# Optimization experiments

Measured on AMD Instinct MI355X. Metric: run time of the kernel, lower is better.

## Reference

```python
import jax, jax.numpy as jnp
import numpy as np

N_NODES = 100000


def gcn_conv(x, W, b, src, dst, n):
    """PyG GCNConv: add self-loops, symmetric degree norm, linear, scatter-add."""
    loop = jnp.arange(n, dtype=src.dtype)
    s = jnp.concatenate([src, loop])  # source nodes (message origin)
    d = jnp.concatenate([dst, loop])  # target nodes (aggregation)
    deg = jax.ops.segment_sum(jnp.ones_like(d, dtype=x.dtype), d, num_segments=n)
    dinv = jnp.where(deg > 0, jax.lax.rsqrt(deg), 0.0)
    norm = dinv[s] * dinv[d]  # [E+N]
    h = x @ W  # [N, out]
    msg = h[s] * norm[:, None]  # [E+N, out]
    return jax.ops.segment_sum(msg, d, num_segments=n) + b


def setup_inputs() -> dict:
    key = jax.random.key(0)
    ks = jax.random.split(key, 8)
    n, e, din, dh, dout = N_NODES, 3200000, 128, 64, 6
    x = jax.random.normal(ks[0], (n, din), dtype=jnp.float32)
    edge_index = jax.random.randint(ks[1], (2, e), 0, n, dtype=jnp.int64)
    sc = lambda f: 1.0 / np.sqrt(f)
    W1 = jax.random.normal(ks[2], (din, dh), dtype=jnp.float32) * sc(din)
    b1 = jnp.zeros((dh,), dtype=jnp.float32)
    W2 = jax.random.normal(ks[3], (dh, dh), dtype=jnp.float32) * sc(dh)
    b2 = jnp.zeros((dh,), dtype=jnp.float32)
    W3 = jax.random.normal(ks[4], (dh, dout), dtype=jnp.float32) * sc(dh)
    b3 = jnp.zeros((dout,), dtype=jnp.float32)
    return {"x": x, "edge_index": edge_index, "W1": W1, "b1": b1,
            "W2": W2, "b2": b2, "W3": W3, "b3": b3}


def reference(x, edge_index, W1, b1, W2, b2, W3, b3):
    n = x.shape[0]
    src, dst = edge_index[0], edge_index[1]
    # eval mode: dropout is identity
    h = jax.nn.relu(gcn_conv(x, W1, b1, src, dst, n))
    h = jax.nn.relu(gcn_conv(h, W2, b2, src, dst, n))
    h = gcn_conv(h, W3, b3, src, dst, n)
    return jax.nn.log_softmax(h, axis=1)
```

## Files before the change

### kernel.cpp

```cpp
#include <hip/hip_runtime.h>
#include <hip/hip_fp16.h>
#include <math.h>


#define WS_ALIGN(x) (((x) + 255) & ~(size_t)255)
#define BKN 256
#define CAP 8960
#define EPT 16
#define BIN_THR 512
#define BIN_CHUNK (BIN_THR * EPT)

typedef _Float16 half8 __attribute__((ext_vector_type(8)));
typedef float floatx4 __attribute__((ext_vector_type(4)));

__global__ __launch_bounds__(BIN_THR) void bin_kernel(
    const int* __restrict__ src, const int* __restrict__ dst,
    int* __restrict__ cur, int* __restrict__ slab, int E, int NB) {
    __shared__ int counts[400];
    const int tid = threadIdx.x;
    const int base = blockIdx.x * BIN_CHUNK + tid * EPT;
    for (int i = tid; i < NB; i += BIN_THR) counts[i] = 0;
    __syncthreads();
    int b[EPT], w[EPT], lpos[EPT];
    #pragma unroll
    for (int k = 0; k < EPT; ++k) {
        int e = base + k;
        if (e < E) {
            int s = src[e], d = dst[e];
            b[k] = d >> 8;
            w[k] = (s << 8) | (d & 255);
        } else b[k] = -1;
    }
    #pragma unroll
    for (int k = 0; k < EPT; ++k)
        if (b[k] >= 0) lpos[k] = atomicAdd(&counts[b[k]], 1);
    __syncthreads();
    for (int i = tid; i < NB; i += BIN_THR) {
        int c = counts[i];
        counts[i] = c ? atomicAdd(&cur[i], c) : 0;
    }
    __syncthreads();
    #pragma unroll
    for (int k = 0; k < EPT; ++k) {
        if (b[k] >= 0) {
            int pos = counts[b[k]] + lpos[k];
            if (pos < CAP) slab[(size_t)b[k] * CAP + pos] = w[k];
        }
    }
}

__global__ __launch_bounds__(512) void bucket_sort_kernel(
    const int* __restrict__ slab, const int* __restrict__ cur,
    int* __restrict__ srcS, int* __restrict__ rowbeg, int* __restrict__ rowend,
    float* __restrict__ dinv, int n) {
    __shared__ int cnt[BKN], s[BKN], cursor[BKN];
    const int b = blockIdx.x, tid = threadIdx.x;
    const int m = min(cur[b], CAP);
    const int* sp = slab + (size_t)b * CAP;
    if (tid < BKN) cnt[tid] = 0;
    __syncthreads();
    for (int j = tid; j < m; j += 512) atomicAdd(&cnt[sp[j] & 255], 1);
    __syncthreads();
    if (tid < BKN) s[tid] = cnt[tid];
    __syncthreads();
    for (int off = 1; off < BKN; off <<= 1) {
        int v = 0;
        if (tid < BKN && tid >= off) v = s[tid - off];
        __syncthreads();
        if (tid < BKN) s[tid] += v;
        __syncthreads();
    }
    if (tid < BKN) {
        int ofs = s[tid] - cnt[tid];
        cursor[tid] = ofs;
        int node = b * BKN + tid;
        if (node < n) {
            rowbeg[node] = b * CAP + ofs;
            rowend[node] = b * CAP + ofs + cnt[tid];
            dinv[node] = rsqrtf((float)(cnt[tid] + 1));
        }
    }
    __syncthreads();
    for (int j = tid; j < m; j += 512) {
        int w = sp[j];
        int p = atomicAdd(&cursor[w & 255], 1);
        srcS[(size_t)b * CAP + p] = w >> 8;
    }
}

template <int K>
__global__ __launch_bounds__(256) void linear_mfma_f32_kernel(
    const float* __restrict__ Xf, const float* __restrict__ W,
    const float* __restrict__ dinv, _Float16* __restrict__ Y, int n) {
    constexpr int KC = K / 32;
    __shared__ _Float16 Bf[KC * 4 * 64 * 8];
    const int tid = threadIdx.x;
    for (int i = tid; i < KC * 4 * 64 * 8; i += 256) {
        int j = i & 7, lane = (i >> 3) & 63, tile = (i >> 9) & 3, kc = i >> 11;
        int k = kc * 32 + ((lane >> 4) << 3) + j;
        int col = tile * 16 + (lane & 15);
        Bf[i] = (_Float16)W[k * 64 + col];
    }
    __syncthreads();
    const int lane = tid & 63, wid = tid >> 6;
    const int base = blockIdx.x * 64 + wid * 16;
    if (base >= n) return;
    const int mrow = lane & 15, quad = lane >> 4;
    const int anode = min(base + mrow, n - 1);
    floatx4 acc[4] = {{0, 0, 0, 0}, {0, 0, 0, 0}, {0, 0, 0, 0}, {0, 0, 0, 0}};
    #pragma unroll
    for (int kc = 0; kc < KC; ++kc) {
        float4 xa = *(const float4*)&Xf[(size_t)anode * K + kc * 32 + quad * 8];
        float4 xb = *(const float4*)&Xf[(size_t)anode * K + kc * 32 + quad * 8 + 4];
        half8 a;
        a[0] = (_Float16)xa.x; a[1] = (_Float16)xa.y; a[2] = (_Float16)xa.z; a[3] = (_Float16)xa.w;
        a[4] = (_Float16)xb.x; a[5] = (_Float16)xb.y; a[6] = (_Float16)xb.z; a[7] = (_Float16)xb.w;
        #pragma unroll
        for (int t = 0; t < 4; ++t) {
            half8 b = *(const half8*)&Bf[((kc * 4 + t) * 64 + lane) * 8];
            acc[t] = __builtin_amdgcn_mfma_f32_16x16x32_f16(a, b, acc[t], 0, 0, 0);
        }
    }
    #pragma unroll
    for (int r = 0; r < 4; ++r) {
        int node = base + quad * 4 + r;
        if (node < n) {
            float di = dinv[node];
            #pragma unroll
            for (int t = 0; t < 4; ++t)
                Y[(size_t)node * 64 + t * 16 + mrow] = (_Float16)(acc[t][r] * di);
        }
    }
}

__global__ __launch_bounds__(256) void linear_mfma_f16_kernel(
    const _Float16* __restrict__ Xh, const float* __restrict__ W,
    const float* __restrict__ dinv, _Float16* __restrict__ Y, int n) {
    constexpr int K = 64, KC = 2;
    __shared__ _Float16 Bf[KC * 4 * 64 * 8];
    const int tid = threadIdx.x;
    for (int i = tid; i < KC * 4 * 64 * 8; i += 256) {
        int j = i & 7, lane = (i >> 3) & 63, tile = (i >> 9) & 3, kc = i >> 11;
        int k = kc * 32 + ((lane >> 4) << 3) + j;
        int col = tile * 16 + (lane & 15);
        Bf[i] = (_Float16)W[k * 64 + col];
    }
    __syncthreads();
    const int lane = tid & 63, wid = tid >> 6;
    const int base = blockIdx.x * 64 + wid * 16;
    if (base >= n) return;
    const int mrow = lane & 15, quad = lane >> 4;
    const int anode = min(base + mrow, n - 1);
    floatx4 acc[4] = {{0, 0, 0, 0}, {0, 0, 0, 0}, {0, 0, 0, 0}, {0, 0, 0, 0}};
    #pragma unroll
    for (int kc = 0; kc < KC; ++kc) {
        half8 a = *(const half8*)&Xh[(size_t)anode * K + kc * 32 + quad * 8];
        #pragma unroll
        for (int t = 0; t < 4; ++t) {
            half8 b = *(const half8*)&Bf[((kc * 4 + t) * 64 + lane) * 8];
            acc[t] = __builtin_amdgcn_mfma_f32_16x16x32_f16(a, b, acc[t], 0, 0, 0);
        }
    }
    #pragma unroll
    for (int r = 0; r < 4; ++r) {
        int node = base + quad * 4 + r;
        if (node < n) {
            float di = dinv[node];
            #pragma unroll
            for (int t = 0; t < 4; ++t)
                Y[(size_t)node * 64 + t * 16 + mrow] = (_Float16)(acc[t][r] * di);
        }
    }
}

__global__ __launch_bounds__(256) void linear3_kernel(const __half* __restrict__ Xh,
                                                      const float* __restrict__ W,
                                                      const float* __restrict__ dinv,
                                                      __half* __restrict__ Y, int n) {
    __shared__ float Wl[64 * 6];
    __shared__ float Xs[32][65];
    const int tid = threadIdx.x;
    for (int i = tid; i < 64 * 6; i += 256) Wl[i] = W[i];
    const int sub = tid >> 3;
    const int feat = tid & 7;
    for (int base = blockIdx.x * 32; base < n; base += gridDim.x * 32) {
        __syncthreads();
        for (int i = tid; i < 32 * 64; i += 256) {
            int r = i >> 6, c = i & 63;
            int node = base + r;
            Xs[r][c] = (node < n) ? __half2float(Xh[(size_t)node * 64 + c]) : 0.f;
        }
        __syncthreads();
        int node = base + sub;
        if (node < n) {
            float r = 0.f;
            if (feat < 6) {
                float acc = 0.f;
                #pragma unroll
                for (int k = 0; k < 64; ++k) acc = fmaf(Xs[sub][k], Wl[k * 6 + feat], acc);
                r = acc * dinv[node];
            }
            Y[(size_t)node * 8 + feat] = __float2half_rn(r);
        }
    }
}

__global__ __launch_bounds__(256) void agg64_kernel(
    const _Float16* __restrict__ Hs, const float* __restrict__ dinv,
    const int* __restrict__ srcS, const int* __restrict__ rowbeg,
    const int* __restrict__ rowend, const float* __restrict__ bias,
    _Float16* __restrict__ Out, int n, int do_relu) {
    const int wave = (blockIdx.x * blockDim.x + threadIdx.x) >> 6;
    const int lane = threadIdx.x & 63;
    if (wave >= n) return;
    const int slot = lane >> 3;
    const int f8 = lane & 7;
    const int beg = rowbeg[wave], end = rowend[wave];
    float acc[8] = {0.f, 0.f, 0.f, 0.f, 0.f, 0.f, 0.f, 0.f};
    int j = beg;
    for (; j + 16 <= end; j += 16) {
        int sA = srcS[j + slot];
        int sB = srcS[j + 8 + slot];
        half8 vA = *(const half8*)&Hs[(size_t)sA * 64 + f8 * 8];
        half8 vB = *(const half8*)&Hs[(size_t)sB * 64 + f8 * 8];
        #pragma unroll
        for (int i = 0; i < 8; ++i) acc[i] += (float)vA[i] + (float)vB[i];
    }
    for (; j < end; j += 8) {
        int jj = j + slot;
        int s = srcS[min(jj, end - 1)];
        half8 v = *(const half8*)&Hs[(size_t)s * 64 + f8 * 8];
        float flag = (jj < end) ? 1.f : 0.f;
        #pragma unroll
        for (int i = 0; i < 8; ++i) acc[i] = fmaf((float)v[i], flag, acc[i]);
    }
    #pragma unroll
    for (int i = 0; i < 8; ++i) {
        acc[i] += __shfl_xor(acc[i], 8);
        acc[i] += __shfl_xor(acc[i], 16);
        acc[i] += __shfl_xor(acc[i], 32);
    }
    half8 self = *(const half8*)&Hs[(size_t)wave * 64 + f8 * 8];
    const float di = dinv[wave];
    float4 b0 = *(const float4*)&bias[f8 * 8];
    float4 b1 = *(const float4*)&bias[f8 * 8 + 4];
    float bb[8] = {b0.x, b0.y, b0.z, b0.w, b1.x, b1.y, b1.z, b1.w};
    half8 o;
    #pragma unroll
    for (int i = 0; i < 8; ++i) {
        float v = (acc[i] + (float)self[i]) * di + bb[i];
        if (do_relu) v = fmaxf(v, 0.f);
        o[i] = (_Float16)v;
    }
    if (slot == 0) *(half8*)&Out[(size_t)wave * 64 + f8 * 8] = o;
}

__global__ __launch_bounds__(256) void agg6_lsm_kernel(
    const __half* __restrict__ Hs6, const float* __restrict__ dinv,
    const int* __restrict__ srcS, const int* __restrict__ rowbeg,
    const int* __restrict__ rowend, const float* __restrict__ bias,
    float* __restrict__ out, int n) {
    const int wave = (blockIdx.x * blockDim.x + threadIdx.x) >> 6;
    const int lane = threadIdx.x & 63;
    if (wave >= n) return;
    const int slot = lane >> 3, f = lane & 7;
    const int beg = rowbeg[wave], end = rowend[wave];
    float part = 0.f;
    for (int j0 = beg; j0 < end; j0 += 8) {
        int j = j0 + slot;
        if (j < end) part += __half2float(Hs6[(size_t)srcS[j] * 8 + f]);
    }
    part += __shfl_xor(part, 8);
    part += __shfl_xor(part, 16);
    part += __shfl_xor(part, 32);
    float bi = (f < 6) ? bias[f] : 0.f;
    float a = (part + __half2float(Hs6[(size_t)wave * 8 + f])) * dinv[wave] + bi;
    float am = (f < 6) ? a : -1e30f;
    float m = am;
    m = fmaxf(m, __shfl_xor(m, 1));
    m = fmaxf(m, __shfl_xor(m, 2));
    m = fmaxf(m, __shfl_xor(m, 4));
    float ex = (f < 6) ? expf(a - m) : 0.f;
    float sum = ex;
    sum += __shfl_xor(sum, 1);
    sum += __shfl_xor(sum, 2);
    sum += __shfl_xor(sum, 4);
    float lse = m + logf(sum);
    if (slot == 0 && f < 6) out[(size_t)wave * 6 + f] = a - lse;
}

extern "C" void kernel_launch(void* const* d_in, const int* in_sizes, int n_in,
                              void* d_out, int out_size, void* d_ws, size_t ws_size,
                              hipStream_t stream) {
    const float* x  = (const float*)d_in[0];
    const int*   ei = (const int*)d_in[1];
    const float* W1 = (const float*)d_in[2];
    const float* b1 = (const float*)d_in[3];
    const float* W2 = (const float*)d_in[4];
    const float* b2 = (const float*)d_in[5];
    const float* W3 = (const float*)d_in[6];
    const float* b3 = (const float*)d_in[7];
    float* out = (float*)d_out;

    const int n = in_sizes[0] / 128;
    const int E = in_sizes[1] / 2;
    const int* src = ei;
    const int* dst = ei + E;
    const int NB = (n + BKN - 1) / BKN;

    char* ws = (char*)d_ws;
    auto carve = [&](size_t bytes) { char* p = ws; ws += WS_ALIGN(bytes); return p; };
    int*      cur    = (int*)     carve((size_t)NB * 4);
    float*    dinv   = (float*)   carve((size_t)n * 4);
    int*      slab   = (int*)     carve((size_t)NB * CAP * 4);
    int*      srcS   = (int*)     carve((size_t)NB * CAP * 4);
    int*      rowbeg = (int*)     carve((size_t)n * 4);
    int*      rowend = (int*)     carve((size_t)n * 4);
    _Float16* hsA    = (_Float16*)carve((size_t)n * 64 * 2 + 4096);
    _Float16* hsB    = (_Float16*)carve((size_t)n * 64 * 2 + 4096);
    __half*   hsC    = (__half*)  carve((size_t)n * 8 * 2);
    (void)ws_size; (void)n_in; (void)out_size;

    hipMemsetAsync(cur, 0, (size_t)NB * 4, stream);
    bin_kernel<<<(E + BIN_CHUNK - 1) / BIN_CHUNK, BIN_THR, 0, stream>>>(src, dst, cur, slab, E, NB);
    bucket_sort_kernel<<<NB, 512, 0, stream>>>(slab, cur, srcS, rowbeg, rowend, dinv, n);

    const int aggGrid = (n + 3) / 4;
    const int linGrid = (n + 63) / 64;

    linear_mfma_f32_kernel<128><<<linGrid, 256, 0, stream>>>(x, W1, dinv, hsA, n);
    agg64_kernel<<<aggGrid, 256, 0, stream>>>(hsA, dinv, srcS, rowbeg, rowend, b1, hsB, n, 1);

    linear_mfma_f16_kernel<<<linGrid, 256, 0, stream>>>(hsB, W2, dinv, hsA, n);
    agg64_kernel<<<aggGrid, 256, 0, stream>>>(hsA, dinv, srcS, rowbeg, rowend, b2, hsB, n, 1);

    linear3_kernel<<<2048, 256, 0, stream>>>((const __half*)hsB, W3, dinv, hsC, n);
    agg6_lsm_kernel<<<aggGrid, 256, 0, stream>>>(hsC, dinv, srcS, rowbeg, rowend, b3, out, n);
}
```

Measured before the change: 374.3 us.

## Accumulate aggregation in packed fp16, shrink buckets, pack row bounds into int2

The aggregation kernel now sums neighbor features with packed half8 vector adds and does its cross-lane reduction on packed halves, where before it converted each value to fp32. This cuts conversion and ALU work in the gather loop. Separately, the binning buckets shrink from 256 to 128 nodes with a smaller capacity and fewer edges per thread, and the row begin/end arrays are merged into one int2 load. The fp16 accumulation over roughly 33 neighbors risks precision loss, and the smaller bucket capacity raises the chance of overflowing a bucket and silently dropping edges.

Measured after the change: 375.9 us. Within noise of the previous version (+0.4%).

```diff
diff --git a/kernel.cpp b/kernel.cpp
--- a/kernel.cpp
+++ b/kernel.cpp
@@ -4,9 +4,9 @@
 
 
 #define WS_ALIGN(x) (((x) + 255) & ~(size_t)255)
-#define BKN 256
-#define CAP 8960
-#define EPT 16
+#define BKN 128
+#define CAP 4608
+#define EPT 8
 #define BIN_THR 512
 #define BIN_CHUNK (BIN_THR * EPT)
 
@@ -16,7 +16,7 @@
 __global__ __launch_bounds__(BIN_THR) void bin_kernel(
     const int* __restrict__ src, const int* __restrict__ dst,
     int* __restrict__ cur, int* __restrict__ slab, int E, int NB) {
-    __shared__ int counts[400];
+    __shared__ int counts[784];
     const int tid = threadIdx.x;
     const int base = blockIdx.x * BIN_CHUNK + tid * EPT;
     for (int i = tid; i < NB; i += BIN_THR) counts[i] = 0;
@@ -27,8 +27,8 @@
         int e = base + k;
         if (e < E) {
             int s = src[e], d = dst[e];
-            b[k] = d >> 8;
-            w[k] = (s << 8) | (d & 255);
+            b[k] = d >> 7;
+            w[k] = (s << 7) | (d & 127);
         } else b[k] = -1;
     }
     #pragma unroll
@@ -51,7 +51,7 @@
 
 __global__ __launch_bounds__(512) void bucket_sort_kernel(
     const int* __restrict__ slab, const int* __restrict__ cur,
-    int* __restrict__ srcS, int* __restrict__ rowbeg, int* __restrict__ rowend,
+    int* __restrict__ srcS, int2* __restrict__ rows,
     float* __restrict__ dinv, int n) {
     __shared__ int cnt[BKN], s[BKN], cursor[BKN];
     const int b = blockIdx.x, tid = threadIdx.x;
@@ -59,7 +59,7 @@
     const int* sp = slab + (size_t)b * CAP;
     if (tid < BKN) cnt[tid] = 0;
     __syncthreads();
-    for (int j = tid; j < m; j += 512) atomicAdd(&cnt[sp[j] & 255], 1);
+    for (int j = tid; j < m; j += 512) atomicAdd(&cnt[sp[j] & (BKN - 1)], 1);
     __syncthreads();
     if (tid < BKN) s[tid] = cnt[tid];
     __syncthreads();
@@ -75,16 +75,15 @@
         cursor[tid] = ofs;
         int node = b * BKN + tid;
         if (node < n) {
-            rowbeg[node] = b * CAP + ofs;
-            rowend[node] = b * CAP + ofs + cnt[tid];
+            rows[node] = make_int2(b * CAP + ofs, b * CAP + ofs + cnt[tid]);
             dinv[node] = rsqrtf((float)(cnt[tid] + 1));
         }
     }
     __syncthreads();
     for (int j = tid; j < m; j += 512) {
         int w = sp[j];
-        int p = atomicAdd(&cursor[w & 255], 1);
-        srcS[(size_t)b * CAP + p] = w >> 8;
+        int p = atomicAdd(&cursor[w & (BKN - 1)], 1);
+        srcS[(size_t)b * CAP + p] = w >> 7;
     }
 }
 
@@ -207,38 +206,44 @@
 
 __global__ __launch_bounds__(256) void agg64_kernel(
     const _Float16* __restrict__ Hs, const float* __restrict__ dinv,
-    const int* __restrict__ srcS, const int* __restrict__ rowbeg,
-    const int* __restrict__ rowend, const float* __restrict__ bias,
-    _Float16* __restrict__ Out, int n, int do_relu) {
+    const int* __restrict__ srcS, const int2* __restrict__ rows,
+    const float* __restrict__ bias, _Float16* __restrict__ Out,
+    int n, int do_relu) {
     const int wave = (blockIdx.x * blockDim.x + threadIdx.x) >> 6;
     const int lane = threadIdx.x & 63;
     if (wave >= n) return;
     const int slot = lane >> 3;
     const int f8 = lane & 7;
-    const int beg = rowbeg[wave], end = rowend[wave];
-    float acc[8] = {0.f, 0.f, 0.f, 0.f, 0.f, 0.f, 0.f, 0.f};
+    const int2 row = rows[wave];
+    const int beg = row.x, end = row.y;
+    half8 hA, hB;
+    #pragma unroll
+    for (int i = 0; i < 8; ++i) { hA[i] = (_Float16)0.f; hB[i] = (_Float16)0.f; }
     int j = beg;
     for (; j + 16 <= end; j += 16) {
         int sA = srcS[j + slot];
         int sB = srcS[j + 8 + slot];
         half8 vA = *(const half8*)&Hs[(size_t)sA * 64 + f8 * 8];
         half8 vB = *(const half8*)&Hs[(size_t)sB * 64 + f8 * 8];
-        #pragma unroll
-        for (int i = 0; i < 8; ++i) acc[i] += (float)vA[i] + (float)vB[i];
+        hA += vA;
+        hB += vB;
     }
     for (; j < end; j += 8) {
         int jj = j + slot;
-        int s = srcS[min(jj, end - 1)];
-        half8 v = *(const half8*)&Hs[(size_t)s * 64 + f8 * 8];
-        float flag = (jj < end) ? 1.f : 0.f;
-        #pragma unroll
-        for (int i = 0; i < 8; ++i) acc[i] = fmaf((float)v[i], flag, acc[i]);
-    }
-    #pragma unroll
-    for (int i = 0; i < 8; ++i) {
-        acc[i] += __shfl_xor(acc[i], 8);
-        acc[i] += __shfl_xor(acc[i], 16);
-        acc[i] += __shfl_xor(acc[i], 32);
+        if (jj < end) {
+            half8 v = *(const half8*)&Hs[(size_t)srcS[jj] * 64 + f8 * 8];
+            hA += v;
+        }
+    }
+    half8 ht = hA + hB;
+    #pragma unroll
+    for (int mask = 8; mask <= 32; mask <<= 1) {
+        int4 ci = *(int4*)&ht, oi;
+        oi.x = __shfl_xor(ci.x, mask);
+        oi.y = __shfl_xor(ci.y, mask);
+        oi.z = __shfl_xor(ci.z, mask);
+        oi.w = __shfl_xor(ci.w, mask);
+        ht += *(half8*)&oi;
     }
     half8 self = *(const half8*)&Hs[(size_t)wave * 64 + f8 * 8];
     const float di = dinv[wave];
@@ -248,23 +253,23 @@
     half8 o;
     #pragma unroll
     for (int i = 0; i < 8; ++i) {
-        float v = (acc[i] + (float)self[i]) * di + bb[i];
-        if (do_relu) v = fmaxf(v, 0.f);
-        o[i] = (_Float16)v;
+        float t = ((float)ht[i] + (float)self[i]) * di + bb[i];
+        if (do_relu) t = fmaxf(t, 0.f);
+        o[i] = (_Float16)t;
     }
     if (slot == 0) *(half8*)&Out[(size_t)wave * 64 + f8 * 8] = o;
 }
 
 __global__ __launch_bounds__(256) void agg6_lsm_kernel(
     const __half* __restrict__ Hs6, const float* __restrict__ dinv,
-    const int* __restrict__ srcS, const int* __restrict__ rowbeg,
-    const int* __restrict__ rowend, const float* __restrict__ bias,
-    float* __restrict__ out, int n) {
+    const int* __restrict__ srcS, const int2* __restrict__ rows,
+    const float* __restrict__ bias, float* __restrict__ out, int n) {
     const int wave = (blockIdx.x * blockDim.x + threadIdx.x) >> 6;
     const int lane = threadIdx.x & 63;
     if (wave >= n) return;
     const int slot = lane >> 3, f = lane & 7;
-    const int beg = rowbeg[wave], end = rowend[wave];
+    const int2 row = rows[wave];
+    const int beg = row.x, end = row.y;
     float part = 0.f;
     for (int j0 = beg; j0 < end; j0 += 8) {
         int j = j0 + slot;
@@ -310,30 +315,29 @@
 
     char* ws = (char*)d_ws;
     auto carve = [&](size_t bytes) { char* p = ws; ws += WS_ALIGN(bytes); return p; };
-    int*      cur    = (int*)     carve((size_t)NB * 4);
-    float*    dinv   = (float*)   carve((size_t)n * 4);
-    int*      slab   = (int*)     carve((size_t)NB * CAP * 4);
-    int*      srcS   = (int*)     carve((size_t)NB * CAP * 4);
-    int*      rowbeg = (int*)     carve((size_t)n * 4);
-    int*      rowend = (int*)     carve((size_t)n * 4);
-    _Float16* hsA    = (_Float16*)carve((size_t)n * 64 * 2 + 4096);
-    _Float16* hsB    = (_Float16*)carve((size_t)n * 64 * 2 + 4096);
-    __half*   hsC    = (__half*)  carve((size_t)n * 8 * 2);
+    int*      cur  = (int*)     carve((size_t)NB * 4);
+    float*    dinv = (float*)   carve((size_t)n * 4);
+    int*      slab = (int*)     carve((size_t)NB * CAP * 4);
+    int*      srcS = (int*)     carve((size_t)NB * CAP * 4);
+    int2*     rows = (int2*)    carve((size_t)n * 8);
+    _Float16* hsA  = (_Float16*)carve((size_t)n * 64 * 2 + 4096);
+    _Float16* hsB  = (_Float16*)carve((size_t)n * 64 * 2 + 4096);
+    _Float16* hsC  = (_Float16*)carve((size_t)n * 8 * 2);
     (void)ws_size; (void)n_in; (void)out_size;
 
     hipMemsetAsync(cur, 0, (size_t)NB * 4, stream);
     bin_kernel<<<(E + BIN_CHUNK - 1) / BIN_CHUNK, BIN_THR, 0, stream>>>(src, dst, cur, slab, E, NB);
-    bucket_sort_kernel<<<NB, 512, 0, stream>>>(slab, cur, srcS, rowbeg, rowend, dinv, n);
+    bucket_sort_kernel<<<NB, 512, 0, stream>>>(slab, cur, srcS, rows, dinv, n);
 
     const int aggGrid = (n + 3) / 4;
     const int linGrid = (n + 63) / 64;
 
     linear_mfma_f32_kernel<128><<<linGrid, 256, 0, stream>>>(x, W1, dinv, hsA, n);
-    agg64_kernel<<<aggGrid, 256, 0, stream>>>(hsA, dinv, srcS, rowbeg, rowend, b1, hsB, n, 1);
+    agg64_kernel<<<aggGrid, 256, 0, stream>>>(hsA, dinv, srcS, rows, b1, hsB, n, 1);
 
     linear_mfma_f16_kernel<<<linGrid, 256, 0, stream>>>(hsB, W2, dinv, hsA, n);
-    agg64_kernel<<<aggGrid, 256, 0, stream>>>(hsA, dinv, srcS, rowbeg, rowend, b2, hsB, n, 1);
-
-    linear3_kernel<<<2048, 256, 0, stream>>>((const __half*)hsB, W3, dinv, hsC, n);
-    agg6_lsm_kernel<<<aggGrid, 256, 0, stream>>>(hsC, dinv, srcS, rowbeg, rowend, b3, out, n);
-}
+    agg64_kernel<<<aggGrid, 256, 0, stream>>>(hsA, dinv, srcS, rows, b2, hsB, n, 1);
+
+    linear3_kernel<<<2048, 256, 0, stream>>>((const __half*)hsB, W3, dinv, (__half*)hsC, n);
+    agg6_lsm_kernel<<<aggGrid, 256, 0, stream>>>((const __half*)hsC, dinv, srcS, rows, b3, out, n);
+}
```
